# Kernel tuning notes

Hardware: AMD Instinct MI355X
Metric: run time of the kernel (lower is better)

Reference implementation:

```python
import jax, jax.numpy as jnp
import numpy as np

B = 32          # graphs per batch
NPG = 4096      # nodes per graph (equal-size graphs -> static shapes)
DEG = 16        # average degree
HID = 16
IN_DIM = 6000
OUT_DIM = 23
N_LAYERS = 15
N_POOL = 3      # int(num_layers/5)
RATIO = 0.6
DIV = 1.0 / 10000.0


def setup_inputs():
    key = jax.random.key(0)
    ks = jax.random.split(key, 12)
    N = B * NPG
    E = N * DEG
    glyph = jax.random.randint(ks[0], (N,), 0, IN_DIM, dtype=jnp.int32)
    xpos = jax.random.randint(ks[1], (N,), 0, 79, dtype=jnp.int32)
    ypos = jax.random.randint(ks[2], (N,), 0, 21, dtype=jnp.int32)
    agent = jax.random.randint(ks[3], (N,), 0, 2, dtype=jnp.int32)
    x = jnp.stack([glyph, xpos, ypos, agent], axis=1)
    # edges confined within each graph (contiguous node blocks per graph)
    offs = jnp.repeat(jnp.arange(B, dtype=jnp.int32) * NPG, NPG * DEG)
    src = jax.random.randint(ks[4], (E,), 0, NPG, dtype=jnp.int32) + offs
    dst = jax.random.randint(ks[5], (E,), 0, NPG, dtype=jnp.int32) + offs
    edge_index = jnp.stack([src, dst])
    batch = jnp.repeat(jnp.arange(B, dtype=jnp.int32), NPG)
    s = 0.1
    embed_glyph = jax.random.normal(ks[6], (IN_DIM, HID)) * s
    embed_agent = jax.random.normal(ks[7], (2, 4)) * s
    first_W = jax.random.normal(ks[8], (HID + 8, HID)) * s
    first_b = jnp.zeros((HID,))
    Ws = jax.random.normal(ks[9], (N_LAYERS, HID, HID)) * s
    bs = jnp.zeros((N_LAYERS, HID))
    pool_ws = jax.random.normal(ks[10], (N_POOL, HID)) * s
    lin_W = jax.random.normal(ks[11], (HID, OUT_DIM)) * s
    lin_b = jnp.zeros((OUT_DIM,))
    return dict(x=x, edge_index=edge_index, batch=batch,
                embed_glyph=embed_glyph, embed_agent=embed_agent,
                first_W=first_W, first_b=first_b, Ws=Ws, bs=bs,
                pool_ws=pool_ws, lin_W=lin_W, lin_b=lin_b)


def _gcn(h, src, dst, emask, W, b):
    # PyG GCNConv: x' = D^{-1/2}(A+I)D^{-1/2} (x W) + b, masked edges removed
    N = h.shape[0]
    h = h @ W
    deg = jax.ops.segment_sum(emask, dst, num_segments=N) + 1.0  # +1 self-loop
    dinv = jax.lax.rsqrt(deg)
    norm = dinv[src] * dinv[dst] * emask          # [E]
    agg = jax.ops.segment_sum(h[src] * norm[:, None], dst, num_segments=N)
    agg = agg + h * (dinv * dinv)[:, None]        # self-loop term: 1/deg
    return agg + b


def _topk_pool(h, src, dst, emask, w, npg):
    # PyG TopKPooling: score = x.w/||w||, keep top ceil(ratio*n) per graph,
    # x_out = x[perm]*tanh(score[perm]); edges kept iff both endpoints kept.
    N = h.shape[0]
    score = (h @ w) / jnp.linalg.norm(w)
    k = int(np.ceil(RATIO * npg))
    _, top_idx = jax.lax.top_k(score.reshape(B, npg), k)   # per-graph top-k
    perm = (top_idx + (jnp.arange(B, dtype=jnp.int32) * npg)[:, None]).reshape(-1)
    h_new = h[perm] * jnp.tanh(score[perm])[:, None]
    newpos = jnp.full((N,), -1, dtype=jnp.int32).at[perm].set(
        jnp.arange(B * k, dtype=jnp.int32))
    ns, nd = newpos[src], newpos[dst]
    valid = (ns >= 0) & (nd >= 0) & (emask > 0.5)
    ns = jnp.where(valid, ns, 0)
    nd = jnp.where(valid, nd, 0)
    new_batch = jnp.repeat(jnp.arange(B, dtype=jnp.int32), k)
    return h_new, ns, nd, valid.astype(h.dtype), new_batch, k


def reference(x, edge_index, batch, embed_glyph, embed_agent,
              first_W, first_b, Ws, bs, pool_ws, lin_W, lin_b):
    fdt = embed_glyph.dtype
    glyph = embed_glyph[x[:, 0]]                 # [N,16]
    agent = embed_agent[x[:, 3]]                 # [N,4]
    xpos = x[:, 1:2].astype(fdt)
    ypos = x[:, 2:3].astype(fdt)
    # faithful to torch.cat((sin,cos), dim=0).reshape(-1,2) (interleaving quirk)
    xe = jnp.concatenate([jnp.sin(xpos * DIV), jnp.cos(xpos * DIV)], axis=0).reshape(-1, 2)
    ye = jnp.concatenate([jnp.sin(ypos * DIV), jnp.cos(ypos * DIV)], axis=0).reshape(-1, 2)
    h = jnp.concatenate([glyph, xe, ye, agent], axis=-1)   # [N,24]
    src, dst = edge_index[0], edge_index[1]
    emask = jnp.ones((src.shape[0],), dtype=fdt)
    h = _gcn(h, src, dst, emask, first_W, first_b)
    npg = NPG
    li = 0
    batch_v = batch
    for blk in range(N_POOL):
        for _ in range(5):
            h = jax.nn.relu(h)
            h = _gcn(h, src, dst, emask, Ws[li], bs[li])
            li += 1
        h, src, dst, emask, batch_v, npg = _topk_pool(h, src, dst, emask, pool_ws[blk], npg)
    counts = jax.ops.segment_sum(jnp.ones((h.shape[0],), fdt), batch_v, num_segments=B)
    pooled = jax.ops.segment_sum(h, batch_v, num_segments=B) / counts[:, None]
    return pooled @ lin_W + lin_b               # [B, OUT_DIM] logits
```

## Files before the change

### kernel.cpp

```cpp
#include <hip/hip_runtime.h>
#include <hip/hip_bf16.h>
#include <math.h>

#define NB 32
#define NPG 4096
#define EPG 65536
#define E_TOT 2097152
#define N0 131072
#define K1 2458
#define K2 1475
#define K3 885
#define ODIM 23
#define DIVC 1e-4f
#define CAP 17408

__device__ __forceinline__ int swz(int nwg) {
  int b = blockIdx.x;
  return (b & 7) * (nwg >> 3) + (b >> 3);
}

__device__ __forceinline__ float4 add4(float4 a, float4 b) {
  return make_float4(a.x + b.x, a.y + b.y, a.z + b.z, a.w + b.w);
}

static __device__ __forceinline__ float posenc(const int* x, int j, int comp) {
  if (j < N0) return sinf((float)x[j * 4 + comp] * DIVC);
  return cosf((float)x[(j - N0) * 4 + comp] * DIVC);
}

__global__ __launch_bounds__(256) void feat_mm_k(
    const int* __restrict__ x, const float* __restrict__ eg,
    const float* __restrict__ ea, const float* __restrict__ fW,
    const float* __restrict__ dinv, float* __restrict__ hw) {
  __shared__ float sW[24 * 16];
  int t = threadIdx.x;
  for (int i = t; i < 24 * 16; i += 256) sW[i] = fW[i];
  __syncthreads();
  int n = swz(N0 / 256) * 256 + t;
  float f[24];
  int g = x[n * 4 + 0];
  int ag = x[n * 4 + 3];
#pragma unroll
  for (int i = 0; i < 16; i++) f[i] = eg[g * 16 + i];
  int j0 = 2 * n, j1 = 2 * n + 1;
  f[16] = posenc(x, j0, 1);
  f[17] = posenc(x, j1, 1);
  f[18] = posenc(x, j0, 2);
  f[19] = posenc(x, j1, 2);
#pragma unroll
  for (int i = 0; i < 4; i++) f[20 + i] = ea[ag * 4 + i];
  float out[16];
#pragma unroll
  for (int o = 0; o < 16; o++) out[o] = 0.f;
#pragma unroll
  for (int i = 0; i < 24; i++) {
    float fi = f[i];
#pragma unroll
    for (int o = 0; o < 16; o++) out[o] += fi * sW[i * 16 + o];
  }
  float dn = dinv[n];
  float4* d4 = (float4*)(hw + (size_t)n * 16);
  d4[0] = make_float4(out[0] * dn, out[1] * dn, out[2] * dn, out[3] * dn);
  d4[1] = make_float4(out[4] * dn, out[5] * dn, out[6] * dn, out[7] * dn);
  d4[2] = make_float4(out[8] * dn, out[9] * dn, out[10] * dn, out[11] * dn);
  d4[3] = make_float4(out[12] * dn, out[13] * dn, out[14] * dn, out[15] * dn);
}

__global__ __launch_bounds__(1024) void cnt0_scan_k(const int* __restrict__ dst,
                                                    int* __restrict__ rp,
                                                    float* __restrict__ dinv) {
  __shared__ int h[NPG];
  __shared__ int sarr[1024];
  int bb = blockIdx.x;
  int g = (bb & 7) * 4 + (bb >> 3);
  int t = threadIdx.x;
  int base = g * NPG;
  for (int i = t; i < NPG; i += 1024) h[i] = 0;
  __syncthreads();
  int ebeg = g * EPG;
  for (int e = ebeg + t; e < ebeg + EPG; e += 1024) atomicAdd(&h[dst[e] - base], 1);
  __syncthreads();
  int h0 = h[4 * t], h1 = h[4 * t + 1], h2 = h[4 * t + 2], h3 = h[4 * t + 3];
  int s = h0 + h1 + h2 + h3;
  sarr[t] = s;
  __syncthreads();
  for (int off = 1; off < 1024; off <<= 1) {
    int v = (t >= off) ? sarr[t - off] : 0;
    __syncthreads();
    sarr[t] += v;
    __syncthreads();
  }
  int ex = sarr[t] - s;
  int gb = g * EPG;
  rp[base + 4 * t + 0] = gb + ex;
  rp[base + 4 * t + 1] = gb + ex + h0;
  rp[base + 4 * t + 2] = gb + ex + h0 + h1;
  rp[base + 4 * t + 3] = gb + ex + h0 + h1 + h2;
  dinv[base + 4 * t + 0] = rsqrtf((float)h0 + 1.f);
  dinv[base + 4 * t + 1] = rsqrtf((float)h1 + 1.f);
  dinv[base + 4 * t + 2] = rsqrtf((float)h2 + 1.f);
  dinv[base + 4 * t + 3] = rsqrtf((float)h3 + 1.f);
  if (g == 31 && t == 1023) rp[N0] = E_TOT;
}

__global__ __launch_bounds__(1024) void fillp2_k(const int* __restrict__ src,
                                                 const int* __restrict__ dst,
                                                 const int* __restrict__ rp,
                                                 int* __restrict__ colx) {
  __shared__ int cur[1024];
  __shared__ int stage[CAP];
  int b = blockIdx.x;
  int xcd = b & 7, idx = b >> 3;
  int g = xcd * 4 + (idx >> 2);
  int r = idx & 3;
  int t = threadIdx.x;
  int base = g * NPG + r * 1024;
  int rbase = rp[base];
  cur[t] = rp[base + t] - rbase;
  int tot = rp[base + 1024] - rbase;
  __syncthreads();
  int ebeg = g * EPG;
  for (int e = ebeg + t; e < ebeg + EPG; e += 1024) {
    int d = dst[e] - base;
    if ((unsigned)d < 1024u) {
      int p = atomicAdd(&cur[d], 1);
      if (p < CAP) stage[p] = src[e];
    }
  }
  __syncthreads();
  for (int i = t; i < tot; i += 1024) colx[rbase + i] = stage[i];
}

__global__ __launch_bounds__(1024) void scan1_k(const int* __restrict__ cnt,
                                                int* __restrict__ rp,
                                                int* __restrict__ bsum) {
  __shared__ int s[1024];
  int t = threadIdx.x;
  int i = blockIdx.x * 1024 + t;
  int v = cnt[i];
  s[t] = v;
  __syncthreads();
  for (int off = 1; off < 1024; off <<= 1) {
    int tv = (t >= off) ? s[t - off] : 0;
    __syncthreads();
    s[t] += tv;
    __syncthreads();
  }
  rp[i] = s[t] - v;
  if (t == 1023) bsum[blockIdx.x] = s[1023];
}

__global__ __launch_bounds__(128) void scan2_k(const int* __restrict__ bsum,
                                               int* __restrict__ boff,
                                               int* __restrict__ rp_tot) {
  __shared__ int s[128];
  int t = threadIdx.x;
  int v = bsum[t];
  s[t] = v;
  __syncthreads();
  for (int off = 1; off < 128; off <<= 1) {
    int tv = (t >= off) ? s[t - off] : 0;
    __syncthreads();
    s[t] += tv;
    __syncthreads();
  }
  boff[t] = s[t] - v;
  if (t == 127) *rp_tot = s[127];
}

__global__ __launch_bounds__(256) void scan3_k(int* __restrict__ rp,
                                               const int* __restrict__ boff,
                                               const int* __restrict__ cnt,
                                               float* __restrict__ dinv) {
  int i = blockIdx.x * 256 + threadIdx.x;
  rp[i] = rp[i] + boff[i >> 10];
  dinv[i] = rsqrtf((float)cnt[i] + 1.f);
}

__global__ __launch_bounds__(256) void fillf_k(const int* __restrict__ rp_old,
                                               const int* __restrict__ col_old,
                                               const int* __restrict__ alive,
                                               const int* __restrict__ rp_new,
                                               int* __restrict__ col_new) {
  int t = threadIdx.x;
  int q = t & 3;
  int nd = t >> 2;
  int n = swz(N0 / 64) * 64 + nd;
  if (!alive[n]) return;
  int p = rp_new[n];
  int beg = rp_old[n], end = rp_old[n + 1];
  int gsh = (t & 63) & ~3;
  for (int e0 = beg; e0 < end; e0 += 4) {
    int e = e0 + q;
    int s = 0;
    bool ok = false;
    if (e < end) {
      s = col_old[e];
      ok = alive[s] != 0;
    }
    unsigned long long bal = __ballot(ok);
    unsigned gb = (unsigned)((bal >> gsh) & 0xFull);
    if (ok) col_new[p + __popc(gb & ((1u << q) - 1u))] = s;
    p += __popc(gb);
  }
}

template <int MODE, bool CA>
__global__ __launch_bounds__(256) void layer_k(
    const float* __restrict__ hw_in, const int* __restrict__ rp,
    const int* __restrict__ colx, const float* __restrict__ dinv,
    const float* __restrict__ bias, const float* __restrict__ Wn,
    const float* __restrict__ pw, const int* __restrict__ alive,
    float* __restrict__ hw_out, float* __restrict__ h_out,
    float* __restrict__ sc) {
  __shared__ float sW[256];
  __shared__ float sh[64][17];
  int t = threadIdx.x;
  int q = t & 3;
  int nd = t >> 2;
  if (MODE == 0) sW[t] = Wn[t];
  int n = swz(N0 / 64) * 64 + nd;
  bool live = (!CA) || (alive[n] != 0);
  float4 b4 = ((const float4*)bias)[q];
  float spw0 = 0.f, spw1 = 0.f, spw2 = 0.f, spw3 = 0.f;
  if (MODE == 1) {
    float4 w4 = ((const float4*)pw)[q];
    float nn = w4.x * w4.x + w4.y * w4.y + w4.z * w4.z + w4.w * w4.w;
    nn += __shfl_xor(nn, 1);
    nn += __shfl_xor(nn, 2);
    float inv = rsqrtf(nn);
    spw0 = w4.x * inv; spw1 = w4.y * inv; spw2 = w4.z * inv; spw3 = w4.w * inv;
  }
  float4 acc = make_float4(0.f, 0.f, 0.f, 0.f);
  float dn = 0.f;
  if (live) {
    dn = dinv[n];
    const float4* hin4 = (const float4*)hw_in;
    int e = rp[n], end = rp[n + 1];
    float4 a0 = make_float4(0.f, 0.f, 0.f, 0.f), a1 = a0, a2 = a0, a3 = a0;
    for (; e + 4 <= end; e += 4) {
      int s0 = colx[e], s1 = colx[e + 1], s2 = colx[e + 2], s3 = colx[e + 3];
      a0 = add4(a0, hin4[(size_t)s0 * 4 + q]);
      a1 = add4(a1, hin4[(size_t)s1 * 4 + q]);
      a2 = add4(a2, hin4[(size_t)s2 * 4 + q]);
      a3 = add4(a3, hin4[(size_t)s3 * 4 + q]);
    }
    for (; e < end; ++e) a0 = add4(a0, hin4[(size_t)colx[e] * 4 + q]);
    float4 self = hin4[(size_t)n * 4 + q];
    acc = add4(add4(add4(a0, a1), add4(a2, a3)), self);
    acc = make_float4(acc.x * dn + b4.x, acc.y * dn + b4.y, acc.z * dn + b4.z,
                      acc.w * dn + b4.w);
  }
  if (MODE == 0) {
    sh[nd][q * 4 + 0] = fmaxf(acc.x, 0.f);
    sh[nd][q * 4 + 1] = fmaxf(acc.y, 0.f);
    sh[nd][q * 4 + 2] = fmaxf(acc.z, 0.f);
    sh[nd][q * 4 + 3] = fmaxf(acc.w, 0.f);
    __syncthreads();
    if (live) {
      float o0 = 0.f, o1 = 0.f, o2 = 0.f, o3 = 0.f;
#pragma unroll
      for (int g = 0; g < 16; g++) {
        float hg = sh[nd][g];
        o0 += hg * sW[g * 16 + q * 4 + 0];
        o1 += hg * sW[g * 16 + q * 4 + 1];
        o2 += hg * sW[g * 16 + q * 4 + 2];
        o3 += hg * sW[g * 16 + q * 4 + 3];
      }
      ((float4*)hw_out)[(size_t)n * 4 + q] =
          make_float4(o0 * dn, o1 * dn, o2 * dn, o3 * dn);
    }
  } else {
    if (live) {
      ((float4*)h_out)[(size_t)n * 4 + q] = acc;
      float part = acc.x * spw0 + acc.y * spw1 + acc.z * spw2 + acc.w * spw3;
      part += __shfl_xor(part, 1);
      part += __shfl_xor(part, 2);
      if (q == 0) sc[n] = part;
    } else if (q == 0) {
      sc[n] = -INFINITY;
    }
  }
}

template <int KC, bool DO_DEG>
__global__ __launch_bounds__(1024) void topk_k(const float* __restrict__ sc,
                                               int* __restrict__ alive,
                                               const int* __restrict__ rp,
                                               const int* __restrict__ colx,
                                               int* __restrict__ degc) {
  __shared__ unsigned keys[NPG];
  __shared__ int hist[NPG];
  __shared__ int sarr[1024];
  __shared__ unsigned abm[NPG / 32];
  __shared__ int sB, sLo, sB2, sLo2, sB3, sLo3;
  int bb = blockIdx.x;
  int b = (bb & 7) * 4 + (bb >> 3);
  int t = threadIdx.x;
  int base = b * NPG;
  for (int i = t; i < NPG; i += 1024) {
    unsigned u = __float_as_uint(sc[base + i]);
    u = (u & 0x80000000u) ? ~u : (u | 0x80000000u);
    keys[i] = ~u;
    alive[base + i] = 0;
    hist[i] = 0;
  }
  if (t < NPG / 32) abm[t] = 0;
  __syncthreads();
  for (int i = t; i < NPG; i += 1024) atomicAdd(&hist[keys[i] >> 20], 1);
  __syncthreads();
  {
    int h0 = hist[4 * t], h1 = hist[4 * t + 1], h2 = hist[4 * t + 2], h3 = hist[4 * t + 3];
    int s = h0 + h1 + h2 + h3;
    sarr[t] = s;
    __syncthreads();
    for (int off = 1; off < 1024; off <<= 1) {
      int v = (t >= off) ? sarr[t - off] : 0;
      __syncthreads();
      sarr[t] += v;
      __syncthreads();
    }
    int ex = sarr[t] - s;
    int e1 = ex + h0, e2 = e1 + h1, e3 = e2 + h2;
    const int R = KC - 1;
    if (R >= ex && R < ex + h0) { sB = 4 * t + 0; sLo = ex; }
    if (R >= e1 && R < e1 + h1) { sB = 4 * t + 1; sLo = e1; }
    if (R >= e2 && R < e2 + h2) { sB = 4 * t + 2; sLo = e2; }
    if (R >= e3 && R < e3 + h3) { sB = 4 * t + 3; sLo = e3; }
  }
  __syncthreads();
  int B = sB, lo = sLo;
  for (int i = t; i < NPG; i += 1024) hist[i] = 0;
  __syncthreads();
  for (int i = t; i < NPG; i += 1024) {
    unsigned k = keys[i];
    if ((int)(k >> 20) == B) atomicAdd(&hist[(k >> 8) & 0xFFFu], 1);
  }
  __syncthreads();
  {
    int h0 = hist[4 * t], h1 = hist[4 * t + 1], h2 = hist[4 * t + 2], h3 = hist[4 * t + 3];
    int s = h0 + h1 + h2 + h3;
    sarr[t] = s;
    __syncthreads();
    for (int off = 1; off < 1024; off <<= 1) {
      int v = (t >= off) ? sarr[t - off] : 0;
      __syncthreads();
      sarr[t] += v;
      __syncthreads();
    }
    int ex = sarr[t] - s;
    int e1 = ex + h0, e2 = e1 + h1, e3 = e2 + h2;
    const int R2 = KC - 1 - lo;
    if (R2 >= ex && R2 < ex + h0) { sB2 = 4 * t + 0; sLo2 = ex; }
    if (R2 >= e1 && R2 < e1 + h1) { sB2 = 4 * t + 1; sLo2 = e1; }
    if (R2 >= e2 && R2 < e2 + h2) { sB2 = 4 * t + 2; sLo2 = e2; }
    if (R2 >= e3 && R2 < e3 + h3) { sB2 = 4 * t + 3; sLo2 = e3; }
  }
  __syncthreads();
  int B2 = sB2, lo2 = sLo2;
  unsigned hi24 = ((unsigned)B << 12) | (unsigned)B2;
  if (t < 256) hist[t] = 0;
  __syncthreads();
  for (int i = t; i < NPG; i += 1024) {
    unsigned k = keys[i];
    if ((k >> 8) == hi24) atomicAdd(&hist[k & 0xFFu], 1);
  }
  __syncthreads();
  int o3 = (t < 256) ? hist[t] : 0;
  for (int off = 1; off < 256; off <<= 1) {
    int v = 0;
    if (t < 256 && t >= off) v = hist[t - off];
    __syncthreads();
    if (t < 256) hist[t] += v;
    __syncthreads();
  }
  {
    const int R3 = KC - 1 - lo - lo2;
    if (t < 256) {
      int ex = hist[t] - o3;
      if (R3 >= ex && R3 < ex + o3) { sB3 = t; sLo3 = ex; }
    }
  }
  __syncthreads();
  unsigned T = (hi24 << 8) | (unsigned)sB3;
  int need = KC - (lo + lo2 + sLo3);
  {
    int i0 = 4 * t;
    unsigned k0 = keys[i0], k1 = keys[i0 + 1], k2 = keys[i0 + 2], k3 = keys[i0 + 3];
    int q0 = (k0 == T), q1 = (k1 == T), q2 = (k2 == T), q3 = (k3 == T);
    int es = q0 + q1 + q2 + q3;
    sarr[t] = es;
    __syncthreads();
    for (int off = 1; off < 1024; off <<= 1) {
      int v = (t >= off) ? sarr[t - off] : 0;
      __syncthreads();
      sarr[t] += v;
      __syncthreads();
    }
    int c = sarr[t] - es;
    bool s0 = (k0 < T) || (q0 && c < need); c += q0;
    bool s1 = (k1 < T) || (q1 && c < need); c += q1;
    bool s2 = (k2 < T) || (q2 && c < need); c += q2;
    bool s3 = (k3 < T) || (q3 && c < need);
    if (s0) { alive[base + i0 + 0] = 1; atomicOr(&abm[(i0 + 0) >> 5], 1u << ((i0 + 0) & 31)); }
    if (s1) { alive[base + i0 + 1] = 1; atomicOr(&abm[(i0 + 1) >> 5], 1u << ((i0 + 1) & 31)); }
    if (s2) { alive[base + i0 + 2] = 1; atomicOr(&abm[(i0 + 2) >> 5], 1u << ((i0 + 2) & 31)); }
    if (s3) { alive[base + i0 + 3] = 1; atomicOr(&abm[(i0 + 3) >> 5], 1u << ((i0 + 3) & 31)); }
  }
  __syncthreads();
  if (DO_DEG) {
    for (int i = t; i < NPG; i += 1024) {
      int dg = 0;
      if ((abm[i >> 5] >> (i & 31)) & 1) {
        int n = base + i;
        int end = rp[n + 1];
        for (int e = rp[n]; e < end; ++e) {
          int s = colx[e] - base;
          dg += (abm[s >> 5] >> (s & 31)) & 1;
        }
      }
      degc[base + i] = dg;
    }
  }
}

__global__ __launch_bounds__(256) void pool_mm_k(const float* __restrict__ h,
                                                 const float* __restrict__ sc,
                                                 const int* __restrict__ alive,
                                                 const float* __restrict__ Wn,
                                                 const float* __restrict__ dinv,
                                                 float* __restrict__ hw_out) {
  __shared__ float sW[256];
  __shared__ float sh[16][17];
  int t = threadIdx.x, f = t & 15, lo = t >> 4;
  sW[t] = Wn[t];
  int n = swz(N0 / 16) * 16 + lo;
  bool live = alive[n] != 0;
  float v = 0.f;
  if (live) v = fmaxf(h[(size_t)n * 16 + f] * tanhf(sc[n]), 0.f);
  sh[lo][f] = v;
  __syncthreads();
  if (live) {
    float o = 0.f;
#pragma unroll
    for (int g = 0; g < 16; g++) o += sh[lo][g] * sW[g * 16 + f];
    hw_out[(size_t)n * 16 + f] = o * dinv[n];
  }
}

__global__ __launch_bounds__(256) void final1_k(const float* __restrict__ h,
                                                const float* __restrict__ sc,
                                                const int* __restrict__ alive,
                                                float* __restrict__ fpart) {
  __shared__ float red[4][16];
  int bb = blockIdx.x;
  int xcd = bb & 7, rest = bb >> 3;
  int g = xcd * 4 + (rest & 3);
  int sub = rest >> 2;
  int t = threadIdx.x;
  int n = g * NPG + sub * 256 + t;
  float w = 0.f;
  if (alive[n]) w = tanhf(sc[n]) * (1.f / (float)K3);
  float v[16];
#pragma unroll
  for (int j = 0; j < 16; j++) v[j] = 0.f;
  if (w != 0.f) {
    const float4* h4 = (const float4*)(h + (size_t)n * 16);
#pragma unroll
    for (int j = 0; j < 4; j++) {
      float4 a = h4[j];
      v[j * 4 + 0] = a.x * w;
      v[j * 4 + 1] = a.y * w;
      v[j * 4 + 2] = a.z * w;
      v[j * 4 + 3] = a.w * w;
    }
  }
#pragma unroll
  for (int off = 1; off < 64; off <<= 1) {
#pragma unroll
    for (int j = 0; j < 16; j++) v[j] += __shfl_xor(v[j], off);
  }
  if ((t & 63) == 0) {
#pragma unroll
    for (int j = 0; j < 16; j++) red[t >> 6][j] = v[j];
  }
  __syncthreads();
  if (t < 16) {
    float s = red[0][t] + red[1][t] + red[2][t] + red[3][t];
    fpart[(g * 16 + sub) * 16 + t] = s;
  }
}

__global__ __launch_bounds__(64) void final2_k(const float* __restrict__ fpart,
                                               const float* __restrict__ lW,
                                               const float* __restrict__ lb,
                                               float* __restrict__ out) {
  __shared__ float ssum[16];
  int g = blockIdx.x;
  int t = threadIdx.x;
  if (t < 16) {
    float s = 0.f;
    for (int j = 0; j < 16; j++) s += fpart[(g * 16 + j) * 16 + t];
    ssum[t] = s;
  }
  __syncthreads();
  if (t < ODIM) {
    float o = lb[t];
#pragma unroll
    for (int q = 0; q < 16; q++) o += ssum[q] * lW[q * ODIM + t];
    out[g * ODIM + t] = o;
  }
}

extern "C" void kernel_launch(void* const* d_in, const int* in_sizes, int n_in,
                              void* d_out, int out_size, void* d_ws, size_t ws_size,
                              hipStream_t stream) {
  const int* x = (const int*)d_in[0];
  const int* ei = (const int*)d_in[1];
  const int* src0 = ei;
  const int* dst0 = ei + E_TOT;
  const float* eg = (const float*)d_in[3];
  const float* ea = (const float*)d_in[4];
  const float* fW = (const float*)d_in[5];
  const float* fb = (const float*)d_in[6];
  const float* Ws = (const float*)d_in[7];
  const float* bs = (const float*)d_in[8];
  const float* pw = (const float*)d_in[9];
  const float* lW = (const float*)d_in[10];
  const float* lb = (const float*)d_in[11];
  float* out = (float*)d_out;

  char* w = (char*)d_ws;
  auto alloc = [&](size_t bytes) {
    char* p = w;
    w += (bytes + 255) & ~(size_t)255;
    return p;
  };
  float* hwA = (float*)alloc((size_t)N0 * 16 * 4);
  float* hwB = (float*)alloc((size_t)N0 * 16 * 4);
  float* hbuf = (float*)alloc((size_t)N0 * 16 * 4);
  int* colA = (int*)alloc((size_t)E_TOT * 4);
  int* colB = (int*)alloc((size_t)E_TOT * 4);
  int* rpA = (int*)alloc((size_t)(N0 + 1) * 4);
  int* rpB = (int*)alloc((size_t)(N0 + 1) * 4);
  int* cnt = (int*)alloc((size_t)N0 * 4);
  int* alive = (int*)alloc((size_t)N0 * 4);
  float* dinv = (float*)alloc((size_t)N0 * 4);
  float* sc = (float*)alloc((size_t)N0 * 4);
  int* bsum = (int*)alloc(128 * 4);
  int* boff = (int*)alloc(128 * 4);
  float* fpart = (float*)alloc((size_t)NB * 16 * 16 * 4);

  auto scan = [&](int* rp) {
    scan1_k<<<N0 / 1024, 1024, 0, stream>>>(cnt, rp, bsum);
    scan2_k<<<1, 128, 0, stream>>>(bsum, boff, rp + N0);
    scan3_k<<<N0 / 256, 256, 0, stream>>>(rp, boff, cnt, dinv);
  };

#define LMID(CA, IN, OUT, RP, COL, BIAS, WNEXT)                               \
  layer_k<0, CA><<<N0 / 64, 256, 0, stream>>>(IN, RP, COL, dinv, BIAS, WNEXT, \
                                              nullptr, alive, OUT, nullptr, nullptr)
#define LEND(CA, IN, RP, COL, BIAS, PW)                                          \
  layer_k<1, CA><<<N0 / 64, 256, 0, stream>>>(IN, RP, COL, dinv, BIAS, nullptr, \
                                              PW, alive, nullptr, hbuf, sc)

  cnt0_scan_k<<<NB, 1024, 0, stream>>>(dst0, rpA, dinv);
  fillp2_k<<<128, 1024, 0, stream>>>(src0, dst0, rpA, colA);
  feat_mm_k<<<N0 / 256, 256, 0, stream>>>(x, eg, ea, fW, dinv, hwA);

  LMID(false, hwA, hwB, rpA, colA, fb, Ws + 0 * 256);
  LMID(false, hwB, hwA, rpA, colA, bs + 0 * 16, Ws + 1 * 256);
  LMID(false, hwA, hwB, rpA, colA, bs + 1 * 16, Ws + 2 * 256);
  LMID(false, hwB, hwA, rpA, colA, bs + 2 * 16, Ws + 3 * 256);
  LMID(false, hwA, hwB, rpA, colA, bs + 3 * 16, Ws + 4 * 256);
  LEND(false, hwB, rpA, colA, bs + 4 * 16, pw + 0);

  topk_k<K1, true><<<NB, 1024, 0, stream>>>(sc, alive, rpA, colA, cnt);
  scan(rpB);
  fillf_k<<<N0 / 64, 256, 0, stream>>>(rpA, colA, alive, rpB, colB);
  pool_mm_k<<<N0 / 16, 256, 0, stream>>>(hbuf, sc, alive, Ws + 5 * 256, dinv, hwA);

  LMID(true, hwA, hwB, rpB, colB, bs + 5 * 16, Ws + 6 * 256);
  LMID(true, hwB, hwA, rpB, colB, bs + 6 * 16, Ws + 7 * 256);
  LMID(true, hwA, hwB, rpB, colB, bs + 7 * 16, Ws + 8 * 256);
  LMID(true, hwB, hwA, rpB, colB, bs + 8 * 16, Ws + 9 * 256);
  LEND(true, hwA, rpB, colB, bs + 9 * 16, pw + 16);

  topk_k<K2, true><<<NB, 1024, 0, stream>>>(sc, alive, rpB, colB, cnt);
  scan(rpA);
  fillf_k<<<N0 / 64, 256, 0, stream>>>(rpB, colB, alive, rpA, colA);
  pool_mm_k<<<N0 / 16, 256, 0, stream>>>(hbuf, sc, alive, Ws + 10 * 256, dinv, hwA);

  LMID(true, hwA, hwB, rpA, colA, bs + 10 * 16, Ws + 11 * 256);
  LMID(true, hwB, hwA, rpA, colA, bs + 11 * 16, Ws + 12 * 256);
  LMID(true, hwA, hwB, rpA, colA, bs + 12 * 16, Ws + 13 * 256);
  LMID(true, hwB, hwA, rpA, colA, bs + 13 * 16, Ws + 14 * 256);
  LEND(true, hwA, rpA, colA, bs + 14 * 16, pw + 32);

  topk_k<K3, false><<<NB, 1024, 0, stream>>>(sc, alive, nullptr, nullptr, nullptr);
  final1_k<<<512, 256, 0, stream>>>(hbuf, sc, alive, fpart);
  final2_k<<<NB, 64, 0, stream>>>(fpart, lW, lb, out);
}
```

Before: 408.6 us.

## Split CSR build into 512-node ranges across more blocks with vectorized edge reads

Replaces the per-graph count+scan kernel (32 blocks) and 4-range fill kernel (128 blocks) with a three-kernel scheme: per-range histogram and local scan over 256 blocks, a tiny offset kernel, and a fill kernel over 256 blocks that only loads src when a dst falls in range. Edge arrays are read as int4. This aims to raise parallelism in the graph-construction prologue, at the cost of each block rescanning its whole graph's dst array and one extra launch. Separately, the layer gather loads four column indices with one lane each and broadcasts them with shuffles, instead of every lane loading all four.

```diff
diff --git a/kernel.cpp b/kernel.cpp
--- a/kernel.cpp
+++ b/kernel.cpp
@@ -12,7 +12,9 @@
 #define K3 885
 #define ODIM 23
 #define DIVC 1e-4f
-#define CAP 17408
+#define RNG 512
+#define NRG 8
+#define CAP2 9088
 
 __device__ __forceinline__ int swz(int nwg) {
   int b = blockIdx.x;
@@ -66,69 +68,99 @@
   d4[3] = make_float4(out[12] * dn, out[13] * dn, out[14] * dn, out[15] * dn);
 }
 
-__global__ __launch_bounds__(1024) void cnt0_scan_k(const int* __restrict__ dst,
-                                                    int* __restrict__ rp,
-                                                    float* __restrict__ dinv) {
-  __shared__ int h[NPG];
-  __shared__ int sarr[1024];
-  int bb = blockIdx.x;
-  int g = (bb & 7) * 4 + (bb >> 3);
-  int t = threadIdx.x;
-  int base = g * NPG;
-  for (int i = t; i < NPG; i += 1024) h[i] = 0;
-  __syncthreads();
-  int ebeg = g * EPG;
-  for (int e = ebeg + t; e < ebeg + EPG; e += 1024) atomicAdd(&h[dst[e] - base], 1);
-  __syncthreads();
-  int h0 = h[4 * t], h1 = h[4 * t + 1], h2 = h[4 * t + 2], h3 = h[4 * t + 3];
-  int s = h0 + h1 + h2 + h3;
-  sarr[t] = s;
-  __syncthreads();
-  for (int off = 1; off < 1024; off <<= 1) {
-    int v = (t >= off) ? sarr[t - off] : 0;
-    __syncthreads();
-    sarr[t] += v;
-    __syncthreads();
-  }
-  int ex = sarr[t] - s;
-  int gb = g * EPG;
-  rp[base + 4 * t + 0] = gb + ex;
-  rp[base + 4 * t + 1] = gb + ex + h0;
-  rp[base + 4 * t + 2] = gb + ex + h0 + h1;
-  rp[base + 4 * t + 3] = gb + ex + h0 + h1 + h2;
-  dinv[base + 4 * t + 0] = rsqrtf((float)h0 + 1.f);
-  dinv[base + 4 * t + 1] = rsqrtf((float)h1 + 1.f);
-  dinv[base + 4 * t + 2] = rsqrtf((float)h2 + 1.f);
-  dinv[base + 4 * t + 3] = rsqrtf((float)h3 + 1.f);
-  if (g == 31 && t == 1023) rp[N0] = E_TOT;
-}
-
-__global__ __launch_bounds__(1024) void fillp2_k(const int* __restrict__ src,
-                                                 const int* __restrict__ dst,
-                                                 const int* __restrict__ rp,
-                                                 int* __restrict__ colx) {
-  __shared__ int cur[1024];
-  __shared__ int stage[CAP];
+__global__ __launch_bounds__(1024) void cntA_k(const int* __restrict__ dst,
+                                               int* __restrict__ rp,
+                                               float* __restrict__ dinv,
+                                               int* __restrict__ rtot) {
+  __shared__ int h[RNG];
+  __shared__ int s[RNG];
   int b = blockIdx.x;
   int xcd = b & 7, idx = b >> 3;
-  int g = xcd * 4 + (idx >> 2);
-  int r = idx & 3;
-  int t = threadIdx.x;
-  int base = g * NPG + r * 1024;
-  int rbase = rp[base];
-  cur[t] = rp[base + t] - rbase;
-  int tot = rp[base + 1024] - rbase;
-  __syncthreads();
-  int ebeg = g * EPG;
-  for (int e = ebeg + t; e < ebeg + EPG; e += 1024) {
-    int d = dst[e] - base;
-    if ((unsigned)d < 1024u) {
-      int p = atomicAdd(&cur[d], 1);
-      if (p < CAP) stage[p] = src[e];
-    }
-  }
-  __syncthreads();
-  for (int i = t; i < tot; i += 1024) colx[rbase + i] = stage[i];
+  int g = xcd * 4 + (idx >> 3);
+  int r = idx & 7;
+  int t = threadIdx.x;
+  int base = g * NPG + r * RNG;
+  if (t < RNG) h[t] = 0;
+  __syncthreads();
+  const int4* d4 = (const int4*)(dst + g * EPG);
+  for (int i = t; i < EPG / 4; i += 1024) {
+    int4 v = d4[i];
+    int d0 = v.x - base, d1 = v.y - base, d2 = v.z - base, d3 = v.w - base;
+    if ((unsigned)d0 < RNG) atomicAdd(&h[d0], 1);
+    if ((unsigned)d1 < RNG) atomicAdd(&h[d1], 1);
+    if ((unsigned)d2 < RNG) atomicAdd(&h[d2], 1);
+    if ((unsigned)d3 < RNG) atomicAdd(&h[d3], 1);
+  }
+  __syncthreads();
+  int v = (t < RNG) ? h[t] : 0;
+  if (t < RNG) {
+    s[t] = v;
+    dinv[base + t] = rsqrtf((float)v + 1.f);
+  }
+  __syncthreads();
+  for (int off = 1; off < RNG; off <<= 1) {
+    int tv = (t < RNG && t >= off) ? s[t - off] : 0;
+    __syncthreads();
+    if (t < RNG) s[t] += tv;
+    __syncthreads();
+  }
+  if (t < RNG) rp[base + t] = s[t] - v;
+  if (t == RNG - 1) rtot[g * NRG + r] = s[RNG - 1];
+}
+
+__global__ __launch_bounds__(256) void cntB_k(const int* __restrict__ rtot,
+                                              int* __restrict__ rbo,
+                                              int* __restrict__ rp) {
+  int t = threadIdx.x;
+  if (t < NB * NRG) {
+    int g = t >> 3, r = t & 7;
+    int s = 0;
+    for (int j = 0; j < r; j++) s += rtot[g * NRG + j];
+    rbo[t] = g * EPG + s;
+  }
+  if (t == 0) rp[N0] = E_TOT;
+}
+
+__global__ __launch_bounds__(1024) void cntC_k(const int* __restrict__ src,
+                                               const int* __restrict__ dst,
+                                               const int* __restrict__ rtot,
+                                               const int* __restrict__ rbo,
+                                               int* __restrict__ rp,
+                                               int* __restrict__ colx) {
+  __shared__ int cur[RNG];
+  __shared__ int stage[CAP2];
+  int b = blockIdx.x;
+  int xcd = b & 7, idx = b >> 3;
+  int g = xcd * 4 + (idx >> 3);
+  int r = idx & 7;
+  int t = threadIdx.x;
+  int base = g * NPG + r * RNG;
+  int gr = g * NRG + r;
+  int rb = rbo[gr];
+  int tot = rtot[gr];
+  if (t < RNG) {
+    int lp = rp[base + t];
+    cur[t] = lp;
+    rp[base + t] = lp + rb;
+  }
+  __syncthreads();
+  const int4* d4 = (const int4*)(dst + g * EPG);
+  const int4* s4 = (const int4*)(src + g * EPG);
+  for (int i = t; i < EPG / 4; i += 1024) {
+    int4 dv = d4[i];
+    int d0 = dv.x - base, d1 = dv.y - base, d2 = dv.z - base, d3 = dv.w - base;
+    bool i0 = (unsigned)d0 < RNG, i1 = (unsigned)d1 < RNG;
+    bool i2 = (unsigned)d2 < RNG, i3 = (unsigned)d3 < RNG;
+    if (i0 | i1 | i2 | i3) {
+      int4 sv = s4[i];
+      if (i0) { int p = atomicAdd(&cur[d0], 1); if (p < CAP2) stage[p] = sv.x; }
+      if (i1) { int p = atomicAdd(&cur[d1], 1); if (p < CAP2) stage[p] = sv.y; }
+      if (i2) { int p = atomicAdd(&cur[d2], 1); if (p < CAP2) stage[p] = sv.z; }
+      if (i3) { int p = atomicAdd(&cur[d3], 1); if (p < CAP2) stage[p] = sv.w; }
+    }
+  }
+  __syncthreads();
+  for (int i = t; i < tot; i += 1024) colx[rb + i] = stage[i];
 }
 
 __global__ __launch_bounds__(1024) void scan1_k(const int* __restrict__ cnt,
@@ -239,7 +271,11 @@
     int e = rp[n], end = rp[n + 1];
     float4 a0 = make_float4(0.f, 0.f, 0.f, 0.f), a1 = a0, a2 = a0, a3 = a0;
     for (; e + 4 <= end; e += 4) {
-      int s0 = colx[e], s1 = colx[e + 1], s2 = colx[e + 2], s3 = colx[e + 3];
+      int myi = colx[e + q];
+      int s0 = __shfl(myi, 0, 4);
+      int s1 = __shfl(myi, 1, 4);
+      int s2 = __shfl(myi, 2, 4);
+      int s3 = __shfl(myi, 3, 4);
       a0 = add4(a0, hin4[(size_t)s0 * 4 + q]);
       a1 = add4(a1, hin4[(size_t)s1 * 4 + q]);
       a2 = add4(a2, hin4[(size_t)s2 * 4 + q]);
@@ -549,6 +585,8 @@
   float* sc = (float*)alloc((size_t)N0 * 4);
   int* bsum = (int*)alloc(128 * 4);
   int* boff = (int*)alloc(128 * 4);
+  int* rtot = (int*)alloc(NB * NRG * 4);
+  int* rbo = (int*)alloc(NB * NRG * 4);
   float* fpart = (float*)alloc((size_t)NB * 16 * 16 * 4);
 
   auto scan = [&](int* rp) {
@@ -564,8 +602,9 @@
   layer_k<1, CA><<<N0 / 64, 256, 0, stream>>>(IN, RP, COL, dinv, BIAS, nullptr, \
                                               PW, alive, nullptr, hbuf, sc)
 
-  cnt0_scan_k<<<NB, 1024, 0, stream>>>(dst0, rpA, dinv);
-  fillp2_k<<<128, 1024, 0, stream>>>(src0, dst0, rpA, colA);
+  cntA_k<<<256, 1024, 0, stream>>>(dst0, rpA, dinv, rtot);
+  cntB_k<<<1, 256, 0, stream>>>(rtot, rbo, rpA);
+  cntC_k<<<256, 1024, 0, stream>>>(src0, dst0, rtot, rbo, rpA, colA);
   feat_mm_k<<<N0 / 256, 256, 0, stream>>>(x, eg, ea, fW, dinv, hwA);
 
   LMID(false, hwA, hwB, rpA, colA, fb, Ws + 0 * 256);
```

Measured after the change: 382.9 us. 1.07x faster.
